# Kernel tuning notes

Hardware: AMD Instinct MI355X
Metric: run time of the kernel (lower is better)

## Reference

```python
import jax, jax.numpy as jnp
import numpy as np

B, N, S, C, NS = 2, 20000, 1024, 256, 16
RADIUS, HMIN, HMAX = 0.05, -0.02, 0.04
NA, ND = 12, 4
EPS = 1e-5  # BatchNorm eps


def setup_inputs() -> dict:
    key = jax.random.key(0)
    ks = jax.random.split(key, 40)
    def rn(k, shape, scale=0.05):
        return jax.random.normal(k, shape, jnp.float32) * scale
    inp = {
        "xyz": jax.random.uniform(ks[0], (B, N, 3), jnp.float32),
        "new_xyz": jax.random.uniform(ks[1], (B, S, 3), jnp.float32),
        "view_rot": jax.random.normal(ks[2], (B, S, 3, 3), jnp.float32),
        "features": jax.random.normal(ks[3], (B, C, N), jnp.float32),
    }
    i = 4
    for li, (o, ci) in enumerate([(512, C + 3), (256, 512), (256, 256)], 1):
        inp[f"mlp{li}_w"] = rn(ks[i], (o, ci)); inp[f"mlp{li}_b"] = rn(ks[i + 1], (o,))
        inp[f"mlp{li}_g"] = jnp.ones((o,), jnp.float32) + rn(ks[i + 2], (o,), 0.01)
        inp[f"mlp{li}_be"] = rn(ks[i + 3], (o,)); i += 4
    for name in ("c1", "c2"):
        inp[f"{name}_w"] = rn(ks[i], (256, 256)); inp[f"{name}_b"] = rn(ks[i + 1], (256,))
        inp[f"{name}_g"] = jnp.ones((256,), jnp.float32) + rn(ks[i + 2], (256,), 0.01)
        inp[f"{name}_be"] = rn(ks[i + 3], (256,)); i += 4
    inp["c3_w"] = rn(ks[i], (NA * ND * 2, 256)); inp["c3_b"] = rn(ks[i + 1], (NA * ND * 2,))
    return inp


def _bn(x, g, be):  # eval-mode BatchNorm with running_mean=0, running_var=1
    return x * (g / jnp.sqrt(1.0 + EPS)) + be


def _forward(xyz, new_xyz, view_rot, features,
             mlp1_w, mlp1_b, mlp1_g, mlp1_be,
             mlp2_w, mlp2_b, mlp2_g, mlp2_be,
             mlp3_w, mlp3_b, mlp3_g, mlp3_be,
             c1_w, c1_b, c1_g, c1_be,
             c2_w, c2_b, c2_g, c2_be,
             c3_w, c3_b):
    # ---- cylinder query (CUDA kernel math: r = rot @ (p - c), cylinder axis = x) ----
    # computed per rotation row to keep intermediates at (B,S,N) each
    comp = []
    for i in range(3):
        rw = view_rot[:, :, i, :]  # (B,S,3)
        comp.append(jnp.einsum('bsj,bpj->bsp', rw, xyz) - jnp.sum(rw * new_xyz, -1)[..., None])
    xr, yr, zr = comp  # each (B,S,N)
    mask = (yr * yr + zr * zr < RADIUS * RADIUS) & (xr > HMIN) & (xr < HMAX)
    # first-NS valid indices per seed (ascending), pad with first valid (0 if none)
    vals = jnp.where(mask, jnp.arange(N, dtype=jnp.int32), N)  # (B,S,N)
    neg_top, _ = jax.lax.top_k(-vals, NS)
    idx = -neg_top  # (B,S,NS) ascending
    first = idx[..., :1]
    first = jnp.where(first >= N, 0, first)
    idx = jnp.where(idx >= N, first, idx)
    # ---- group ----
    b_ix = jnp.arange(B)[:, None, None]
    g_xyz = xyz[b_ix, idx]                                  # (B,S,NS,3)
    g_feat = jnp.transpose(features, (0, 2, 1))[b_ix, idx]  # (B,S,NS,C)
    diff = (g_xyz - new_xyz[:, :, None, :]) / RADIUS        # normalize_xyz
    rot_xyz = jnp.einsum('bsnk,bskj->bsnj', diff, view_rot)  # rotate_xyz: diff @ rot
    h = jnp.concatenate([rot_xyz, g_feat], axis=-1)          # (B,S,NS,C+3)
    # ---- SharedMLP (1x1 conv2d + BN + ReLU) ----
    for w, bb, g, be in ((mlp1_w, mlp1_b, mlp1_g, mlp1_be),
                         (mlp2_w, mlp2_b, mlp2_g, mlp2_be),
                         (mlp3_w, mlp3_b, mlp3_g, mlp3_be)):
        h = jax.nn.relu(_bn(jnp.einsum('bsnc,oc->bsno', h, w) + bb, g, be))
    h = h.max(axis=2)  # max-pool over samples -> (B,S,256)
    # ---- pointwise conv1d head ----
    h = jax.nn.relu(_bn(jnp.einsum('bsc,oc->bso', h, c1_w) + c1_b, c1_g, c1_be))
    h = jax.nn.relu(_bn(jnp.einsum('bsc,oc->bso', h, c2_w) + c2_b, c2_g, c2_be))
    out = jnp.einsum('bsc,oc->bso', h, c3_w) + c3_b  # (B,S,NA*ND*2)
    return out


def reference(xyz, new_xyz, view_rot, features,
              mlp1_w, mlp1_b, mlp1_g, mlp1_be,
              mlp2_w, mlp2_b, mlp2_g, mlp2_be,
              mlp3_w, mlp3_b, mlp3_g, mlp3_be,
              c1_w, c1_b, c1_g, c1_be,
              c2_w, c2_b, c2_g, c2_be,
              c3_w, c3_b):
    return _forward(xyz, new_xyz, view_rot, features,
                    mlp1_w, mlp1_b, mlp1_g, mlp1_be,
                    mlp2_w, mlp2_b, mlp2_g, mlp2_be,
                    mlp3_w, mlp3_b, mlp3_g, mlp3_be,
                    c1_w, c1_b, c1_g, c1_be,
                    c2_w, c2_b, c2_g, c2_be,
                    c3_w, c3_b)
```

## Files before the change

kernel.cpp:

```cpp
#include <hip/hip_runtime.h>
#include <hip/hip_bf16.h>
#include <stdint.h>
#include <limits.h>

#define B_   2
#define N_   20000
#define S_   1024
#define C_   256
#define NS_  16
#define NQ   (B_ * S_)
#define M_   (NQ * NS_)
#define K1P  288
#define O1   512
#define O2   256
#define O3   256
#define OUTC 96

#define R2C   ((float)(0.05 * 0.05))
#define HMINC ((float)(-0.02))
#define HMAXC ((float)(0.04))

#define GDIM   16
#define GCELLS (GDIM * GDIM * GDIM)
#define GTOT   (B_ * GCELLS)
#define CAP    256

__device__ __forceinline__ unsigned short f2b(float f) {
    union { float f; unsigned int i; } x; x.f = f;
    unsigned int r = x.i + 0x7FFFu + ((x.i >> 16) & 1u);
    return (unsigned short)(r >> 16);
}

__device__ __forceinline__ void gl16(const unsigned short* g, unsigned short* l) {
    __builtin_amdgcn_global_load_lds(
        (const __attribute__((address_space(1))) unsigned int*)g,
        (__attribute__((address_space(3))) unsigned int*)l,
        16, 0, 0);
}

__global__ __launch_bounds__(256) void prep_w123z(const float* __restrict__ m1w,
                                                  const float* __restrict__ m2w,
                                                  const float* __restrict__ m3w,
                                                  unsigned short* __restrict__ w1p,
                                                  unsigned short* __restrict__ w2p,
                                                  unsigned short* __restrict__ w3p,
                                                  int* __restrict__ gcnt) {
    int i = blockIdx.x * 256 + threadIdx.x;
    if (i < GTOT) gcnt[i] = 0;
    if (i < O1 * K1P) {
        int o = i / K1P, k = i - o * K1P;
        float v = 0.0f;
        if (k < 256)      v = m1w[o * 259 + 3 + k];
        else if (k < 259) v = m1w[o * 259 + (k - 256)];
        w1p[i] = (k < 259) ? f2b(v) : (unsigned short)0;
    } else if (i < O1 * K1P + O2 * 512) {
        int j = i - O1 * K1P;
        w2p[j] = f2b(m2w[j]);
    } else if (i < O1 * K1P + O2 * 512 + O3 * 256) {
        int j = i - O1 * K1P - O2 * 512;
        w3p[j] = f2b(m3w[j]);
    }
}

__global__ __launch_bounds__(256) void transpose_feat(const float* __restrict__ feat,
                                                      unsigned short* __restrict__ feat_t) {
    __shared__ float tile[32][33];
    int n0 = blockIdx.x * 32, c0 = blockIdx.y * 32, b = blockIdx.z;
    int t = threadIdx.x;
    int nl = t & 31;
#pragma unroll
    for (int i = 0; i < 4; ++i) {
        int cl = (t >> 5) + i * 8;
        tile[cl][nl] = feat[((size_t)(b * C_ + c0 + cl)) * N_ + n0 + nl];
    }
    __syncthreads();
    int nr = t >> 3, c4 = (t & 7) * 4;
    ushort4 v;
    v.x = f2b(tile[c4 + 0][nr]);
    v.y = f2b(tile[c4 + 1][nr]);
    v.z = f2b(tile[c4 + 2][nr]);
    v.w = f2b(tile[c4 + 3][nr]);
    *(ushort4*)(feat_t + ((size_t)(b * N_ + n0 + nr)) * C_ + c0 + c4) = v;
}

__device__ __forceinline__ int cell_of(float px, float py, float pz, int b) {
    int cx = (int)(px * (float)GDIM); cx = min(GDIM - 1, max(0, cx));
    int cy = (int)(py * (float)GDIM); cy = min(GDIM - 1, max(0, cy));
    int cz = (int)(pz * (float)GDIM); cz = min(GDIM - 1, max(0, cz));
    return b * GCELLS + cz * (GDIM * GDIM) + cy * GDIM + cx;
}

__global__ __launch_bounds__(256) void grid_count(const float* __restrict__ xyz,
                                                  int* __restrict__ counts) {
    int i = blockIdx.x * 256 + threadIdx.x;
    if (i < B_ * N_) {
        int b = i / N_;
        const float* p = xyz + (size_t)i * 3;
        atomicAdd(counts + cell_of(p[0], p[1], p[2], b), 1);
    }
}

__global__ __launch_bounds__(256) void grid_scan(const int* __restrict__ counts,
                                                 int* __restrict__ start,
                                                 int* __restrict__ cursor) {
    __shared__ int part[256];
    int t = threadIdx.x;
    int local[32];
    int s = 0;
#pragma unroll
    for (int i = 0; i < 32; ++i) { local[i] = counts[t * 32 + i]; s += local[i]; }
    part[t] = s;
    __syncthreads();
    if (t == 0) {
        int r = 0;
        for (int i = 0; i < 256; ++i) { int x = part[i]; part[i] = r; r += x; }
    }
    __syncthreads();
    int r = part[t];
#pragma unroll
    for (int i = 0; i < 32; ++i) {
        start[t * 32 + i] = r;
        cursor[t * 32 + i] = r;
        r += local[i];
    }
    if (t == 255) start[GTOT] = r;
}

__global__ __launch_bounds__(256) void grid_scatter(const float* __restrict__ xyz,
                                                    int* __restrict__ cursor,
                                                    float4* __restrict__ sorted) {
    int i = blockIdx.x * 256 + threadIdx.x;
    if (i < B_ * N_) {
        int b = i / N_, n = i - b * N_;
        const float* p = xyz + (size_t)i * 3;
        float px = p[0], py = p[1], pz = p[2];
        int pos = atomicAdd(cursor + cell_of(px, py, pz, b), 1);
        sorted[pos] = make_float4(px, py, pz, __int_as_float(n));
    }
}

__device__ __forceinline__ void sort16(int* buf, int cnt, int lane) {
    asm volatile("s_waitcnt lgkmcnt(0)" ::: "memory");
    __builtin_amdgcn_sched_barrier(0);
    int a0 = INT_MAX, a1 = INT_MAX, a2 = INT_MAX, a3 = INT_MAX;
    if (lane < cnt)       a0 = buf[lane];
    if (lane + 64 < cnt)  a1 = buf[lane + 64];
    if (lane + 128 < cnt) a2 = buf[lane + 128];
    if (lane + 192 < cnt) a3 = buf[lane + 192];
#pragma unroll
    for (int t = 0; t < NS_; ++t) {
        int v = a0, sl = 0;
        if (a1 < v) { v = a1; sl = 1; }
        if (a2 < v) { v = a2; sl = 2; }
        if (a3 < v) { v = a3; sl = 3; }
        int pp = (sl << 6) | lane;
#pragma unroll
        for (int off = 1; off < 64; off <<= 1) {
            int ov = __shfl_xor(v, off);
            int op = __shfl_xor(pp, off);
            if (ov < v) { v = ov; pp = op; }
        }
        if ((pp & 63) == lane) {
            int s = pp >> 6;
            if (s == 0) a0 = INT_MAX;
            else if (s == 1) a1 = INT_MAX;
            else if (s == 2) a2 = INT_MAX;
            else a3 = INT_MAX;
        }
        if (lane == 0) buf[t] = v;
    }
    asm volatile("s_waitcnt lgkmcnt(0)" ::: "memory");
    __builtin_amdgcn_sched_barrier(0);
}

#define SCAN_SPAN(SS, EE)                                                    \
    for (int base = (SS); base < (EE); base += 64) {                         \
        int p = base + lane;                                                 \
        bool m = false; int n = 0;                                           \
        if (p < (EE)) {                                                      \
            float4 v = sorted[p];                                            \
            n = __float_as_int(v.w);                                         \
            float px = v.x, py = v.y, pz = v.z;                              \
            float xr = ((R[0]*px + R[1]*py) + R[2]*pz) - dq0;                \
            float yr = ((R[3]*px + R[4]*py) + R[5]*pz) - dq1;                \
            float zr = ((R[6]*px + R[7]*py) + R[8]*pz) - dq2;                \
            m = ((yr*yr + zr*zr) < R2C) && (xr > HMINC) && (xr < HMAXC);     \
        }                                                                    \
        unsigned long long bal = __ballot(m);                                \
        if (m) {                                                             \
            int pos = cnt + __popcll(bal & ((1ull << lane) - 1ull));         \
            buf[pos] = n;                                                    \
        }                                                                    \
        int h = __popcll(bal);                                               \
        cnt += h; tot += h;                                                  \
        if (cnt > CAP - 64) { sort16(buf, cnt, lane); cnt = NS_; }           \
    }

__global__ __launch_bounds__(256) void cyl_query_grid(const float* __restrict__ xyz,
                                                      const float* __restrict__ new_xyz,
                                                      const float* __restrict__ view_rot,
                                                      const float4* __restrict__ sorted,
                                                      const int* __restrict__ cell_start,
                                                      int* __restrict__ idx_out) {
#pragma clang fp contract(off)
    int w = threadIdx.x >> 6, lane = threadIdx.x & 63;
    int q = blockIdx.x;
    int b = q >> 10;

    __shared__ int bufs[4][CAP];
    __shared__ int tots[4];
    int* buf = bufs[w];

    const float* nq = new_xyz + (size_t)q * 3;
    float qx = nq[0], qy = nq[1], qz = nq[2];
    const float* rp = view_rot + (size_t)q * 9;
    float R[9];
#pragma unroll
    for (int i = 0; i < 9; ++i) R[i] = rp[i];
    float dq0 = (R[0]*qx + R[1]*qy) + R[2]*qz;
    float dq1 = (R[3]*qx + R[4]*qy) + R[5]*qz;
    float dq2 = (R[6]*qx + R[7]*qy) + R[8]*qz;

    int x0 = 0, x1 = GDIM - 1, y0 = 0, y1 = GDIM - 1, z0 = 0, z1 = GDIM - 1;
    bool ok = false;
    {
        float det = R[0]*(R[4]*R[8]-R[5]*R[7])
                  - R[1]*(R[3]*R[8]-R[5]*R[6])
                  + R[2]*(R[3]*R[7]-R[4]*R[6]);
        float adet = fabsf(det);
        if (adet > 1e-30f) {
            ok = true;
            float id = 1.0f / det;
            float m00 = (R[4]*R[8]-R[5]*R[7])*id, m01 = (R[2]*R[7]-R[1]*R[8])*id, m02 = (R[1]*R[5]-R[2]*R[4])*id;
            float m10 = (R[5]*R[6]-R[3]*R[8])*id, m11 = (R[0]*R[8]-R[2]*R[6])*id, m12 = (R[2]*R[3]-R[0]*R[5])*id;
            float m20 = (R[3]*R[7]-R[4]*R[6])*id, m21 = (R[1]*R[6]-R[0]*R[7])*id, m22 = (R[0]*R[4]-R[1]*R[3])*id;
            const float mid = 0.5f * (HMINC + HMAXC);
            const float hh  = 0.5f * (HMAXC - HMINC);
            float cx = qx + m00 * mid, cy = qy + m10 * mid, cz = qz + m20 * mid;
            float ex = hh * fabsf(m00) + 0.05f * sqrtf(m01*m01 + m02*m02);
            float ey = hh * fabsf(m10) + 0.05f * sqrtf(m11*m11 + m12*m12);
            float ez = hh * fabsf(m20) + 0.05f * sqrtf(m21*m21 + m22*m22);
            ex = ex * 1.002f + 1e-3f;
            ey = ey * 1.002f + 1e-3f;
            ez = ez * 1.002f + 1e-3f;
            x0 = (int)fmaxf(0.0f, fminf((float)(GDIM - 1), floorf((cx - ex) * (float)GDIM)));
            x1 = (int)fmaxf(0.0f, fminf((float)(GDIM - 1), floorf((cx + ex) * (float)GDIM)));
            y0 = (int)fmaxf(0.0f, fminf((float)(GDIM - 1), floorf((cy - ey) * (float)GDIM)));
            y1 = (int)fmaxf(0.0f, fminf((float)(GDIM - 1), floorf((cy + ey) * (float)GDIM)));
            z0 = (int)fmaxf(0.0f, fminf((float)(GDIM - 1), floorf((cz - ez) * (float)GDIM)));
            z1 = (int)fmaxf(0.0f, fminf((float)(GDIM - 1), floorf((cz + ez) * (float)GDIM)));
        }
    }

    int nx = x1 - x0 + 1, ny = y1 - y0 + 1, nz = z1 - z0 + 1;
    bool heavy = (!ok) || (ny * nz > 256) || (nx * ny * nz > 512);

    int cnt = 0, tot = 0;
    int cbase = b * GCELLS;

    if (!heavy) {
        int NR = ny * nz;
        int nr_w = (NR - w + 3) >> 2;
        int sl = 0, el = 0;
        if (lane < nr_w) {
            int ri = w + (lane << 2);
            int zi = ri / ny;
            int yi = ri - zi * ny;
            int cid = cbase + (z0 + zi) * (GDIM * GDIM) + (y0 + yi) * GDIM;
            sl = cell_start[cid + x0];
            el = cell_start[cid + x1 + 1];
        }
        for (int j = 0; j < nr_w; ++j) {
            int s = __shfl(sl, j), e = __shfl(el, j);
            SCAN_SPAN(s, e)
        }
    } else {
        int bstart = b * N_;
        int s = bstart + w * (N_ / 4);
        int e = s + (N_ / 4);
        for (int base = s; base < e && cnt < NS_; base += 512) {
            float px[8], py[8], pz[8];
#pragma unroll
            for (int k = 0; k < 8; ++k) {
                int p = base + k * 64 + lane;
                int pc = min(p, e - 1);
                const float* pp = xyz + (size_t)pc * 3;
                px[k] = pp[0]; py[k] = pp[1]; pz[k] = pp[2];
            }
#pragma unroll
            for (int k = 0; k < 8; ++k) {
                if (cnt >= NS_) break;
                int p = base + k * 64 + lane;
                bool m = false;
                if (p < e) {
                    float xr = ((R[0]*px[k] + R[1]*py[k]) + R[2]*pz[k]) - dq0;
                    float yr = ((R[3]*px[k] + R[4]*py[k]) + R[5]*pz[k]) - dq1;
                    float zr = ((R[6]*px[k] + R[7]*py[k]) + R[8]*pz[k]) - dq2;
                    m = ((yr*yr + zr*zr) < R2C) && (xr > HMINC) && (xr < HMAXC);
                }
                unsigned long long bal = __ballot(m);
                if (m) {
                    int pos = cnt + __popcll(bal & ((1ull << lane) - 1ull));
                    buf[pos] = p - bstart;
                }
                int h = __popcll(bal);
                cnt += h; tot += h;
            }
        }
    }

    sort16(buf, cnt, lane);
    if (lane == 0) tots[w] = tot;
    __syncthreads();

    if (w == 0) {
        int cand = bufs[lane >> 4][lane & 15];
        int myv = INT_MAX;
#pragma unroll
        for (int t = 0; t < NS_; ++t) {
            int v = cand, pp = lane;
#pragma unroll
            for (int off = 1; off < 64; off <<= 1) {
                int ov = __shfl_xor(v, off);
                int op = __shfl_xor(pp, off);
                if (ov < v) { v = ov; pp = op; }
            }
            if (lane == t) myv = v;
            if (pp == lane) cand = INT_MAX;
        }
        int tt = tots[0] + tots[1] + tots[2] + tots[3];
        int total = tt < NS_ ? tt : NS_;
        int first = (tt > 0) ? __shfl(myv, 0) : 0;
        if (lane < NS_)
            idx_out[q * NS_ + lane] = (lane < total) ? myv : first;
    }
}

__global__ __launch_bounds__(256) void build_h0(const float* __restrict__ xyz,
                                                const float* __restrict__ new_xyz,
                                                const float* __restrict__ view_rot,
                                                const unsigned short* __restrict__ feat_t,
                                                const int* __restrict__ idxs,
                                                unsigned short* __restrict__ h0) {
#pragma clang fp contract(off)
    int q = blockIdx.x;
    int b = q >> 10;
    int t = threadIdx.x;
    __shared__ int pidx[NS_];
    if (t < NS_) pidx[t] = idxs[q * NS_ + t];
    __syncthreads();

#pragma unroll
    for (int pass = 0; pass < 2; ++pass) {
        int n = pass * 8 + (t >> 5);
        int p = pidx[n];
        uint4 v = *(const uint4*)(feat_t + ((size_t)(b * N_ + p)) * C_ + (t & 31) * 8);
        *(uint4*)(h0 + (size_t)(q * NS_ + n) * K1P + (t & 31) * 8) = v;
    }

    if (t < NS_) {
        int n = t, p = pidx[n];
        const float* pp = xyz + ((size_t)b * N_ + p) * 3;
        const float* nq = new_xyz + (size_t)q * 3;
        float dx = (pp[0] - nq[0]) / 0.05f;
        float dy = (pp[1] - nq[1]) / 0.05f;
        float dz = (pp[2] - nq[2]) / 0.05f;
        const float* rp = view_rot + (size_t)q * 9;
        float r0 = (dx * rp[0] + dy * rp[3]) + dz * rp[6];
        float r1 = (dx * rp[1] + dy * rp[4]) + dz * rp[7];
        float r2 = (dx * rp[2] + dy * rp[5]) + dz * rp[8];
        size_t row = (size_t)(q * NS_ + n) * K1P;
        h0[row + 256] = f2b(r0);
        h0[row + 257] = f2b(r1);
        h0[row + 258] = f2b(r2);
    }
    for (int e = t; e < NS_ * 29; e += 256) {
        int n = e / 29, c = 259 + (e - n * 29);
        h0[(size_t)(q * NS_ + n) * K1P + c] = 0;
    }
}

typedef float f32x4 __attribute__((ext_vector_type(4)));
typedef short s16x8 __attribute__((ext_vector_type(8)));

__global__ __launch_bounds__(256) void gemm_bn_relu(const unsigned short* __restrict__ A,
                                                    const unsigned short* __restrict__ W,
                                                    const float* __restrict__ bias,
                                                    const float* __restrict__ gam,
                                                    const float* __restrict__ bet,
                                                    unsigned short* __restrict__ out,
                                                    int M, int Nn, int K) {
    __shared__ __align__(16) unsigned short As[128 * 32];
    __shared__ __align__(16) unsigned short Bs[128 * 32];
    int tid  = threadIdx.x;
    int lane = tid & 63, wave = tid >> 6;
    int m0 = blockIdx.x * 128, n0 = blockIdx.y * 128;
    int wm = (wave >> 1) * 64, wn = (wave & 1) * 64;

    f32x4 acc[4][4] = {};

    for (int k0 = 0; k0 < K; k0 += 32) {
        __syncthreads();
#pragma unroll
        for (int j = 0; j < 2; ++j) {
            int e = j * 256 + tid;
            int r = e >> 2, c8 = (e & 3) << 3;
            gl16(A + (size_t)(m0 + r) * K + k0 + c8, &As[e * 8]);
            gl16(W + (size_t)(n0 + r) * K + k0 + c8, &Bs[e * 8]);
        }
        __syncthreads();

        int kq = (lane >> 4) * 8, rr = lane & 15;
        s16x8 af[4], bfr[4];
#pragma unroll
        for (int i = 0; i < 4; ++i) af[i]  = *(const s16x8*)&As[(wm + i * 16 + rr) * 32 + kq];
#pragma unroll
        for (int j = 0; j < 4; ++j) bfr[j] = *(const s16x8*)&Bs[(wn + j * 16 + rr) * 32 + kq];
#pragma unroll
        for (int i = 0; i < 4; ++i)
#pragma unroll
            for (int j = 0; j < 4; ++j)
                acc[i][j] = __builtin_amdgcn_mfma_f32_16x16x32_bf16(af[i], bfr[j], acc[i][j], 0, 0, 0);
    }

    float inv = 1.0f / sqrtf(1.0f + 1e-5f);
    int col = lane & 15, rq = (lane >> 4) * 4;
#pragma unroll
    for (int j = 0; j < 4; ++j) {
        int n = n0 + wn + j * 16 + col;
        float sc = gam[n] * inv;
        float tb = bias[n] * sc + bet[n];
#pragma unroll
        for (int i = 0; i < 4; ++i) {
            int mbase = m0 + wm + i * 16 + rq;
#pragma unroll
            for (int r = 0; r < 4; ++r) {
                float v = acc[i][j][r] * sc + tb;
                v = fmaxf(v, 0.0f);
                out[(size_t)(mbase + r) * Nn + n] = f2b(v);
            }
        }
    }
}

__global__ __launch_bounds__(512) void gemm23_pool(const unsigned short* __restrict__ A,
                                                   const unsigned short* __restrict__ W2,
                                                   const float* __restrict__ bias2,
                                                   const float* __restrict__ gam2,
                                                   const float* __restrict__ bet2,
                                                   const unsigned short* __restrict__ W3,
                                                   const float* __restrict__ bias3,
                                                   const float* __restrict__ gam3,
                                                   const float* __restrict__ bet3,
                                                   const float* __restrict__ c1w,
                                                   const float* __restrict__ c2w,
                                                   const float* __restrict__ c3w,
                                                   unsigned short* __restrict__ wprep,
                                                   unsigned short* __restrict__ hp) {
    __shared__ __align__(16) unsigned short As[128 * 32];
    __shared__ __align__(16) unsigned short Bs[256 * 32];
    __shared__ __align__(16) unsigned short H2[128 * 256];
    int tid = threadIdx.x, lane = tid & 63, wave = tid >> 6;
    int m0 = blockIdx.x * 128;
    int wm = (wave >> 1) * 32, wn = (wave & 1) * 128;
    int kq = (lane >> 4) * 8, rr = lane & 15;
    int col = lane & 15, rq = (lane >> 4) * 4;
    float inv = 1.0f / sqrtf(1.0f + 1e-5f);

    f32x4 acc[2][8] = {};

    for (int k0 = 0; k0 < 512; k0 += 32) {
        __syncthreads();
        {
            int r = tid >> 2, c8 = (tid & 3) << 3;
            gl16(A + (size_t)(m0 + r) * 512 + k0 + c8, &As[tid * 8]);
        }
#pragma unroll
        for (int j = 0; j < 2; ++j) {
            int e = j * 512 + tid;
            int r = e >> 2, c8 = (e & 3) << 3;
            gl16(W2 + (size_t)r * 512 + k0 + c8, &Bs[e * 8]);
        }
        __syncthreads();
        s16x8 af[2], bf[8];
#pragma unroll
        for (int i = 0; i < 2; ++i) af[i] = *(const s16x8*)&As[(wm + i * 16 + rr) * 32 + kq];
#pragma unroll
        for (int j = 0; j < 8; ++j) bf[j] = *(const s16x8*)&Bs[(wn + j * 16 + rr) * 32 + kq];
#pragma unroll
        for (int i = 0; i < 2; ++i)
#pragma unroll
            for (int j = 0; j < 8; ++j)
                acc[i][j] = __builtin_amdgcn_mfma_f32_16x16x32_bf16(af[i], bf[j], acc[i][j], 0, 0, 0);
    }

    {
        int e0 = blockIdx.x * 768;
        for (int e = e0 + tid; e < e0 + 768; e += 512) {
            int l = e >> 16, j = e & 65535, row = j >> 8, kcol = j & 255;
            float v;
            if (l == 0)      v = c1w[j];
            else if (l == 1) v = c2w[j];
            else             v = (row < OUTC) ? c3w[row * 256 + kcol] : 0.0f;
            int c = kcol & 127;
            wprep[l * 65536 + (kcol >> 7) * 32768 + row * 128 + (c ^ ((row & 7) << 3))] = f2b(v);
        }
    }

#pragma unroll
    for (int j = 0; j < 8; ++j) {
        int n = wn + j * 16 + col;
        float sc = gam2[n] * inv;
        float tb = bias2[n] * sc + bet2[n];
#pragma unroll
        for (int i = 0; i < 2; ++i) {
#pragma unroll
            for (int r = 0; r < 4; ++r) {
                int row = wm + i * 16 + rq + r;
                float v = fmaxf(acc[i][j][r] * sc + tb, 0.0f);
                *(unsigned short*)((char*)H2 + row * 512 + ((2 * n) ^ ((row & 7) << 4))) = f2b(v);
            }
        }
    }

#pragma unroll
    for (int i = 0; i < 2; ++i)
#pragma unroll
        for (int j = 0; j < 8; ++j) acc[i][j] = (f32x4){0.f, 0.f, 0.f, 0.f};

    for (int k0 = 0; k0 < 256; k0 += 32) {
        __syncthreads();
#pragma unroll
        for (int j = 0; j < 2; ++j) {
            int e = j * 512 + tid;
            int r = e >> 2, c8 = (e & 3) << 3;
            gl16(W3 + (size_t)r * 256 + k0 + c8, &Bs[e * 8]);
        }
        __syncthreads();
        s16x8 af[2], bf[8];
#pragma unroll
        for (int i = 0; i < 2; ++i) {
            int row = wm + i * 16 + rr;
            af[i] = *(const s16x8*)((const char*)H2 + row * 512 + ((2 * (k0 + kq)) ^ ((row & 7) << 4)));
        }
#pragma unroll
        for (int j = 0; j < 8; ++j) bf[j] = *(const s16x8*)&Bs[(wn + j * 16 + rr) * 32 + kq];
#pragma unroll
        for (int i = 0; i < 2; ++i)
#pragma unroll
            for (int j = 0; j < 8; ++j)
                acc[i][j] = __builtin_amdgcn_mfma_f32_16x16x32_bf16(af[i], bf[j], acc[i][j], 0, 0, 0);
    }

    int qbase = (m0 + wm) >> 4;
#pragma unroll
    for (int j = 0; j < 8; ++j) {
        int n = wn + j * 16 + col;
        float sc = gam3[n] * inv;
        float tb = bias3[n] * sc + bet3[n];
#pragma unroll
        for (int i = 0; i < 2; ++i) {
            float mx = 0.0f;
#pragma unroll
            for (int r = 0; r < 4; ++r)
                mx = fmaxf(mx, acc[i][j][r] * sc + tb);
            mx = fmaxf(mx, __shfl_xor(mx, 16, 64));
            mx = fmaxf(mx, __shfl_xor(mx, 32, 64));
            if (lane < 16)
                hp[(size_t)(qbase + i) * 256 + n] = f2b(mx);
        }
    }
}

__device__ __forceinline__ void head_gemm(const unsigned short* __restrict__ act,
                                          unsigned short* __restrict__ Ws,
                                          const unsigned short* __restrict__ Wp,
                                          int tid, int lane, int wn, f32x4 acc[4][4]) {
    int kq = (lane >> 4) * 8, rr = lane & 15;
    for (int h = 0; h < 2; ++h) {
        __syncthreads();
        const unsigned short* src = Wp + h * 32768;
#pragma unroll
        for (int p = 0; p < 16; ++p)
            gl16(src + (p * 256 + tid) * 8, Ws + (p * 256 + tid) * 8);
        __syncthreads();
        int k0 = h * 128;
#pragma unroll
        for (int kk = 0; kk < 128; kk += 32) {
            s16x8 af[4], bf[4];
#pragma unroll
            for (int i = 0; i < 4; ++i) {
                int row = i * 16 + rr;
                af[i] = *(const s16x8*)((const char*)act + row * 512 + ((2 * (k0 + kk + kq)) ^ ((row & 7) << 4)));
            }
#pragma unroll
            for (int j = 0; j < 4; ++j) {
                int row = wn + j * 16 + rr;
                bf[j] = *(const s16x8*)&Ws[row * 128 + ((kk + kq) ^ ((row & 7) << 3))];
            }
#pragma unroll
            for (int i = 0; i < 4; ++i)
#pragma unroll
                for (int j = 0; j < 4; ++j)
                    acc[i][j] = __builtin_amdgcn_mfma_f32_16x16x32_bf16(af[i], bf[j], acc[i][j], 0, 0, 0);
        }
    }
}

__global__ __launch_bounds__(256) void head_fused(const unsigned short* __restrict__ hp,
                                                  const unsigned short* __restrict__ wp,
                                                  const float* __restrict__ c1b,
                                                  const float* __restrict__ c1g, const float* __restrict__ c1be,
                                                  const float* __restrict__ c2b,
                                                  const float* __restrict__ c2g, const float* __restrict__ c2be,
                                                  const float* __restrict__ c3b,
                                                  float* __restrict__ out) {
    __shared__ __align__(16) unsigned short actA[64 * 256];
    __shared__ __align__(16) unsigned short actB[64 * 256];
    __shared__ __align__(16) unsigned short Ws[256 * 128];
    int tid = threadIdx.x, lane = tid & 63, wave = tid >> 6;
    int q0 = blockIdx.x * 64;
    int wn = wave * 64, col = lane & 15, rq = (lane >> 4) * 4;
    float inv = 1.0f / sqrtf(1.0f + 1e-5f);

#pragma unroll
    for (int j = 0; j < 8; ++j) {
        int c = j * 256 + tid;
        int row = c >> 5, cb = c & 31;
        uint4 v = *(const uint4*)(hp + (size_t)(q0 + row) * 256 + cb * 8);
        *(uint4*)((char*)actA + row * 512 + (((unsigned)cb << 4) ^ ((row & 7) << 4))) = v;
    }

    f32x4 acc[4][4];

#pragma unroll
    for (int i = 0; i < 4; ++i)
#pragma unroll
        for (int j = 0; j < 4; ++j) acc[i][j] = (f32x4){0.f, 0.f, 0.f, 0.f};
    head_gemm(actA, Ws, wp, tid, lane, wn, acc);
#pragma unroll
    for (int j = 0; j < 4; ++j) {
        int n = wn + j * 16 + col;
        float sc = c1g[n] * inv, tb = c1b[n] * sc + c1be[n];
#pragma unroll
        for (int i = 0; i < 4; ++i)
#pragma unroll
            for (int r = 0; r < 4; ++r) {
                int row = i * 16 + rq + r;
                float v = fmaxf(acc[i][j][r] * sc + tb, 0.0f);
                *(unsigned short*)((char*)actB + row * 512 + ((2 * n) ^ ((row & 7) << 4))) = f2b(v);
            }
    }

#pragma unroll
    for (int i = 0; i < 4; ++i)
#pragma unroll
        for (int j = 0; j < 4; ++j) acc[i][j] = (f32x4){0.f, 0.f, 0.f, 0.f};
    head_gemm(actB, Ws, wp + 65536, tid, lane, wn, acc);
#pragma unroll
    for (int j = 0; j < 4; ++j) {
        int n = wn + j * 16 + col;
        float sc = c2g[n] * inv, tb = c2b[n] * sc + c2be[n];
#pragma unroll
        for (int i = 0; i < 4; ++i)
#pragma unroll
            for (int r = 0; r < 4; ++r) {
                int row = i * 16 + rq + r;
                float v = fmaxf(acc[i][j][r] * sc + tb, 0.0f);
                *(unsigned short*)((char*)actA + row * 512 + ((2 * n) ^ ((row & 7) << 4))) = f2b(v);
            }
    }

#pragma unroll
    for (int i = 0; i < 4; ++i)
#pragma unroll
        for (int j = 0; j < 4; ++j) acc[i][j] = (f32x4){0.f, 0.f, 0.f, 0.f};
    head_gemm(actA, Ws, wp + 131072, tid, lane, wn, acc);
#pragma unroll
    for (int j = 0; j < 4; ++j) {
        int n = wn + j * 16 + col;
        if (n < OUTC) {
            float bb = c3b[n];
#pragma unroll
            for (int i = 0; i < 4; ++i)
#pragma unroll
                for (int r = 0; r < 4; ++r)
                    out[(size_t)(q0 + i * 16 + rq + r) * OUTC + n] = acc[i][j][r] + bb;
        }
    }
}

extern "C" void kernel_launch(void* const* d_in, const int* in_sizes, int n_in,
                              void* d_out, int out_size, void* d_ws, size_t ws_size,
                              hipStream_t stream) {
    const float* xyz      = (const float*)d_in[0];
    const float* new_xyz  = (const float*)d_in[1];
    const float* view_rot = (const float*)d_in[2];
    const float* feat     = (const float*)d_in[3];
    const float* m1w = (const float*)d_in[4];
    const float* m1b = (const float*)d_in[5];
    const float* m1g = (const float*)d_in[6];
    const float* m1be= (const float*)d_in[7];
    const float* m2w = (const float*)d_in[8];
    const float* m2b = (const float*)d_in[9];
    const float* m2g = (const float*)d_in[10];
    const float* m2be= (const float*)d_in[11];
    const float* m3w = (const float*)d_in[12];
    const float* m3b = (const float*)d_in[13];
    const float* m3g = (const float*)d_in[14];
    const float* m3be= (const float*)d_in[15];
    const float* c1w = (const float*)d_in[16];
    const float* c1b = (const float*)d_in[17];
    const float* c1g = (const float*)d_in[18];
    const float* c1be= (const float*)d_in[19];
    const float* c2w = (const float*)d_in[20];
    const float* c2b = (const float*)d_in[21];
    const float* c2g = (const float*)d_in[22];
    const float* c2be= (const float*)d_in[23];
    const float* c3w = (const float*)d_in[24];
    const float* c3b = (const float*)d_in[25];

    char* ws = (char*)d_ws;
    int*            idxs = (int*)ws;
    unsigned short* w1p  = (unsigned short*)(ws + 131072);
    unsigned short* w2p  = (unsigned short*)(ws + 425984);
    unsigned short* w3p  = (unsigned short*)(ws + 688128);
    unsigned short* h0   = (unsigned short*)(ws + 819200);
    unsigned short* hp   = (unsigned short*)(ws + 819200);
    unsigned short* wprep= (unsigned short*)(ws + 1867776);
    char*           h1b  = ws + 19693568;
    unsigned short* h1   = (unsigned short*)h1b;
    unsigned short* featt= (unsigned short*)(h1b + 12582912);
    float4*         srt  = (float4*)(h1b + 0);
    int*            gcnt = (int*)(h1b + 640000);
    int*            gsta = (int*)(h1b + 672768);
    int*            gcur = (int*)(h1b + 705552);

    hipLaunchKernelGGL(prep_w123z, dim3((O1 * K1P + O2 * 512 + O3 * 256) / 256), dim3(256), 0, stream,
                       m1w, m2w, m3w, w1p, w2p, w3p, gcnt);
    hipLaunchKernelGGL(grid_count, dim3((B_ * N_ + 255) / 256), dim3(256), 0, stream, xyz, gcnt);
    hipLaunchKernelGGL(grid_scan, dim3(1), dim3(256), 0, stream, gcnt, gsta, gcur);
    hipLaunchKernelGGL(grid_scatter, dim3((B_ * N_ + 255) / 256), dim3(256), 0, stream, xyz, gcur, srt);
    hipLaunchKernelGGL(cyl_query_grid, dim3(NQ), dim3(256), 0, stream,
                       xyz, new_xyz, view_rot, srt, gsta, idxs);
    hipLaunchKernelGGL(transpose_feat, dim3(N_ / 32, C_ / 32, B_), dim3(256), 0, stream, feat, featt);
    hipLaunchKernelGGL(build_h0, dim3(NQ), dim3(256), 0, stream, xyz, new_xyz, view_rot, featt, idxs, h0);
    hipLaunchKernelGGL(gemm_bn_relu, dim3(M_ / 128, O1 / 128), dim3(256), 0, stream,
                       h0, w1p, m1b, m1g, m1be, h1, M_, O1, K1P);
    hipLaunchKernelGGL(gemm23_pool, dim3(M_ / 128), dim3(512), 0, stream,
                       h1, w2p, m2b, m2g, m2be, w3p, m3b, m3g, m3be,
                       c1w, c2w, c3w, wprep, hp);
    hipLaunchKernelGGL(head_fused, dim3(NQ / 64), dim3(256), 0, stream,
                       hp, wprep, c1b, c1g, c1be, c2b, c2g, c2be, c3b, (float*)d_out);
}
```

Baseline: 259.9 us.

## Cull grid cells per row against the cylinder and drop the brute-force fallback

The cylinder query now tests each grid cell in a row against the rotated cylinder, using a conservative bound on the cell's extent. It then scans only the x-range of cells that can hold a hit, not the whole bounding-box row. The brute-force linear-scan path for large or degenerate bounding boxes is removed, so every query goes through the grid, up to all 16x16 rows. This cuts wasted point tests in the grid path. In exchange, wide-footprint queries lose the early exit the linear scan had after finding enough neighbours, and every lane pays a per-cell culling loop.

```diff
diff --git a/kernel.cpp b/kernel.cpp
--- a/kernel.cpp
+++ b/kernel.cpp
@@ -196,8 +196,7 @@
         if (cnt > CAP - 64) { sort16(buf, cnt, lane); cnt = NS_; }           \
     }
 
-__global__ __launch_bounds__(256) void cyl_query_grid(const float* __restrict__ xyz,
-                                                      const float* __restrict__ new_xyz,
+__global__ __launch_bounds__(256) void cyl_query_grid(const float* __restrict__ new_xyz,
                                                       const float* __restrict__ view_rot,
                                                       const float4* __restrict__ sorted,
                                                       const int* __restrict__ cell_start,
@@ -222,14 +221,12 @@
     float dq2 = (R[6]*qx + R[7]*qy) + R[8]*qz;
 
     int x0 = 0, x1 = GDIM - 1, y0 = 0, y1 = GDIM - 1, z0 = 0, z1 = GDIM - 1;
-    bool ok = false;
     {
         float det = R[0]*(R[4]*R[8]-R[5]*R[7])
                   - R[1]*(R[3]*R[8]-R[5]*R[6])
                   + R[2]*(R[3]*R[7]-R[4]*R[6]);
         float adet = fabsf(det);
         if (adet > 1e-30f) {
-            ok = true;
             float id = 1.0f / det;
             float m00 = (R[4]*R[8]-R[5]*R[7])*id, m01 = (R[2]*R[7]-R[1]*R[8])*id, m02 = (R[1]*R[5]-R[2]*R[4])*id;
             float m10 = (R[5]*R[6]-R[3]*R[8])*id, m11 = (R[0]*R[8]-R[2]*R[6])*id, m12 = (R[2]*R[3]-R[0]*R[5])*id;
@@ -252,60 +249,47 @@
         }
     }
 
-    int nx = x1 - x0 + 1, ny = y1 - y0 + 1, nz = z1 - z0 + 1;
-    bool heavy = (!ok) || (ny * nz > 256) || (nx * ny * nz > 512);
-
+    int ny = y1 - y0 + 1, nz = z1 - z0 + 1;
     int cnt = 0, tot = 0;
     int cbase = b * GCELLS;
 
-    if (!heavy) {
+    {
         int NR = ny * nz;
         int nr_w = (NR - w + 3) >> 2;
+        const float inv16 = 0.0625f, half = 0.03125f;
+        float ax = (fabsf(R[0]) + fabsf(R[1]) + fabsf(R[2])) * half + 2e-4f;
+        float ay = (fabsf(R[3]) + fabsf(R[4]) + fabsf(R[5])) * half + 2e-4f;
+        float az = (fabsf(R[6]) + fabsf(R[7]) + fabsf(R[8])) * half + 2e-4f;
         int sl = 0, el = 0;
         if (lane < nr_w) {
             int ri = w + (lane << 2);
             int zi = ri / ny;
             int yi = ri - zi * ny;
-            int cid = cbase + (z0 + zi) * (GDIM * GDIM) + (y0 + yi) * GDIM;
-            sl = cell_start[cid + x0];
-            el = cell_start[cid + x1 + 1];
+            float cy0 = (y0 + yi + 0.5f) * inv16;
+            float cz0 = (z0 + zi + 0.5f) * inv16;
+            float cx0 = (x0 + 0.5f) * inv16;
+            float xr = (R[0]*cx0 + R[1]*cy0) + R[2]*cz0 - dq0;
+            float yr = (R[3]*cx0 + R[4]*cy0) + R[5]*cz0 - dq1;
+            float zr = (R[6]*cx0 + R[7]*cy0) + R[8]*cz0 - dq2;
+            float sx = R[0] * inv16, sy = R[3] * inv16, sz = R[6] * inv16;
+            int xa = 1 << 28, xb = -1;
+            for (int cx = x0; cx <= x1; ++cx) {
+                bool px = (xr + ax > HMINC) && (xr - ax < HMAXC);
+                float dy = fmaxf(fabsf(yr) - ay, 0.0f);
+                float dz = fmaxf(fabsf(zr) - az, 0.0f);
+                bool pr = (dy*dy + dz*dz) < (R2C + 1e-5f);
+                if (px && pr) { if (cx < xa) xa = cx; xb = cx; }
+                xr += sx; yr += sy; zr += sz;
+            }
+            if (xb >= xa) {
+                int cid = cbase + (z0 + zi) * (GDIM * GDIM) + (y0 + yi) * GDIM;
+                sl = cell_start[cid + xa];
+                el = cell_start[cid + xb + 1];
+            }
         }
         for (int j = 0; j < nr_w; ++j) {
             int s = __shfl(sl, j), e = __shfl(el, j);
             SCAN_SPAN(s, e)
-        }
-    } else {
-        int bstart = b * N_;
-        int s = bstart + w * (N_ / 4);
-        int e = s + (N_ / 4);
-        for (int base = s; base < e && cnt < NS_; base += 512) {
-            float px[8], py[8], pz[8];
-#pragma unroll
-            for (int k = 0; k < 8; ++k) {
-                int p = base + k * 64 + lane;
-                int pc = min(p, e - 1);
-                const float* pp = xyz + (size_t)pc * 3;
-                px[k] = pp[0]; py[k] = pp[1]; pz[k] = pp[2];
-            }
-#pragma unroll
-            for (int k = 0; k < 8; ++k) {
-                if (cnt >= NS_) break;
-                int p = base + k * 64 + lane;
-                bool m = false;
-                if (p < e) {
-                    float xr = ((R[0]*px[k] + R[1]*py[k]) + R[2]*pz[k]) - dq0;
-                    float yr = ((R[3]*px[k] + R[4]*py[k]) + R[5]*pz[k]) - dq1;
-                    float zr = ((R[6]*px[k] + R[7]*py[k]) + R[8]*pz[k]) - dq2;
-                    m = ((yr*yr + zr*zr) < R2C) && (xr > HMINC) && (xr < HMAXC);
-                }
-                unsigned long long bal = __ballot(m);
-                if (m) {
-                    int pos = cnt + __popcll(bal & ((1ull << lane) - 1ull));
-                    buf[pos] = p - bstart;
-                }
-                int h = __popcll(bal);
-                cnt += h; tot += h;
-            }
         }
     }
 
@@ -742,7 +726,7 @@
     hipLaunchKernelGGL(grid_scan, dim3(1), dim3(256), 0, stream, gcnt, gsta, gcur);
     hipLaunchKernelGGL(grid_scatter, dim3((B_ * N_ + 255) / 256), dim3(256), 0, stream, xyz, gcur, srt);
     hipLaunchKernelGGL(cyl_query_grid, dim3(NQ), dim3(256), 0, stream,
-                       xyz, new_xyz, view_rot, srt, gsta, idxs);
+                       new_xyz, view_rot, srt, gsta, idxs);
     hipLaunchKernelGGL(transpose_feat, dim3(N_ / 32, C_ / 32, B_), dim3(256), 0, stream, feat, featt);
     hipLaunchKernelGGL(build_h0, dim3(NQ), dim3(256), 0, stream, xyz, new_xyz, view_rot, featt, idxs, h0);
     hipLaunchKernelGGL(gemm_bn_relu, dim3(M_ / 128, O1 / 128), dim3(256), 0, stream,
```

Measured after the change: 257.5 us. About the same (-0.9%).
